# Kernel optimization log

Measured on AMD Instinct MI355X. Metric: run time of the kernel, lower is better.

## Reference

```python
import jax, jax.numpy as jnp
import numpy as np

V, E, D = 100000, 128, 60  # vocab, embedding_size, d_alpha
B, J, M, P = 512, 101, 50, 5120
EPS = 1e-6


def setup_inputs() -> dict:
    key = jax.random.key(0)
    ks = jax.random.split(key, 12)
    s = 0.5 / E
    inp = {
        'batch_titems': jax.random.randint(ks[0], (B, J), 0, V),
        'batch_citems': jax.random.randint(ks[1], (B, M), 0, V),
        'batch_pad_ids': jax.random.randint(ks[2], (2, P), 0, M),
        't_emb': jax.random.uniform(ks[3], (V, E), jnp.float32, -s, s),
        'c_emb': jax.random.uniform(ks[4], (V, E), jnp.float32, -s, s),
        'Ac_w': jax.random.normal(ks[5], (D, E), jnp.float32) * 0.05,
        'Ac_b': jnp.zeros((D,), jnp.float32),
        'At_w': jax.random.normal(ks[6], (D, E), jnp.float32) * 0.05,
        'At_b': jnp.zeros((D,), jnp.float32),
        'Bc_w': jax.random.normal(ks[7], (E, E), jnp.float32) * 0.05,
        'Bc_b': jnp.zeros((E,), jnp.float32),
        'R_w': jax.random.normal(ks[8], (E, E), jnp.float32) * 0.05,
        'R_b': jnp.zeros((E,), jnp.float32),
    }
    return inp


def reference(batch_titems, batch_citems, batch_pad_ids, t_emb, c_emb,
              Ac_w, Ac_b, At_w, At_b, Bc_w, Bc_b, R_w, R_b):
    v = t_emb[batch_titems]            # [B, J, E] target item vectors
    u = c_emb[batch_citems]            # [B, M, E] context item vectors
    tp = v @ At_w.T + At_b             # [B, J, D]
    cp = u @ Ac_w.T + Ac_b             # [B, M, D]
    # cosine similarity with torch eps clamp on norms
    dot = jnp.einsum('bjd,bmd->bjm', tp, cp)
    nt = jnp.maximum(jnp.linalg.norm(tp, axis=-1), EPS)  # [B, J]
    nc = jnp.maximum(jnp.linalg.norm(cp, axis=-1), EPS)  # [B, M]
    cos = dot / (nt[:, :, None] * nc[:, None, :])        # [B, J, M]
    # pad mask: (batch, context-pos) pairs masked across all J target rows
    mask = jnp.zeros((cos.shape[0], cos.shape[2]), bool)
    mask = mask.at[batch_pad_ids[0], batch_pad_ids[1]].set(True)
    scores = jnp.where(mask[:, None, :], -jnp.inf, cos)
    attn = jax.nn.softmax(scores, axis=-1)               # [B, J, M]
    bu = u @ Bc_w.T + Bc_b                               # [B, M, E]
    alpha = jnp.einsum('bjm,bme->bje', attn, bu)         # [B, J, E]
    return alpha @ R_w.T + R_b                           # [B, J, E]
```

## Files before the change

kernel.cpp:

```cpp
#include <hip/hip_runtime.h>

typedef unsigned short u16;
typedef unsigned int   u32;
typedef short bf8 __attribute__((ext_vector_type(8)));
typedef float f4  __attribute__((ext_vector_type(4)));

#define NB   512
#define NJ   101
#define NM   50
#define NE   128
#define ND   60
#define NP   5120
#define NT   512
#define EPSV 1e-6f

#define U_B    0
#define T_B    17408
#define C_B    33536
#define H_B    42752
#define NT2_B  61184
#define NC2_B  61632
#define MSK_B  61888
#define ARENA  62144

__device__ __forceinline__ u16 f2bh(float f) {
    return (u16)((__float_as_uint(f) + 0x8000u) >> 16);
}
__device__ __forceinline__ u32 pk2(float a, float b) {
    u32 ia = __float_as_uint(a) + 0x8000u;
    u32 ib = __float_as_uint(b) + 0x8000u;
    return (ia >> 16) | (ib & 0xFFFF0000u);
}
__device__ __forceinline__ bf8 gfrag(const float* p) {
    const float4* q = (const float4*)p;
    float4 x = q[0], y = q[1];
    union { u32 u[4]; bf8 v; } r;
    r.u[0] = pk2(x.x, x.y); r.u[1] = pk2(x.z, x.w);
    r.u[2] = pk2(y.x, y.y); r.u[3] = pk2(y.z, y.w);
    return r.v;
}

__global__ __launch_bounds__(128) void w2_kernel(
    const float* __restrict__ Bc_w, const float* __restrict__ Bc_b,
    const float* __restrict__ R_w,  const float* __restrict__ R_b,
    u16* __restrict__ w2t, float* __restrict__ rb2)
{
    const int e = blockIdx.x, k = threadIdx.x;
    const float* Rrow = R_w + e * NE;
    float a0 = 0.f, a1 = 0.f, a2 = 0.f, a3 = 0.f;
    #pragma unroll 8
    for (int j = 0; j < NE; j += 4) {
        a0 += Rrow[j]     * Bc_w[j * NE + k];
        a1 += Rrow[j + 1] * Bc_w[(j + 1) * NE + k];
        a2 += Rrow[j + 2] * Bc_w[(j + 2) * NE + k];
        a3 += Rrow[j + 3] * Bc_w[(j + 3) * NE + k];
    }
    w2t[e * NE + k] = f2bh((a0 + a1) + (a2 + a3));
    float c = Bc_b[k] * Rrow[k];
    for (int o = 32; o; o >>= 1) c += __shfl_xor(c, o, 64);
    __shared__ float part[2];
    if ((k & 63) == 0) part[k >> 6] = c;
    __syncthreads();
    if (k == 0) rb2[e] = part[0] + part[1] + R_b[e];
}

__global__ __launch_bounds__(NT, 4) void aitv_kernel(
    const int* __restrict__ titems, const int* __restrict__ citems,
    const int* __restrict__ pad_ids,
    const float* __restrict__ t_emb, const float* __restrict__ c_emb,
    const float* __restrict__ Ac_w,  const float* __restrict__ Ac_b,
    const float* __restrict__ At_w,  const float* __restrict__ At_b,
    const u16* __restrict__ w2t,     const float* __restrict__ rb2g,
    float* __restrict__ out)
{
    const int b    = blockIdx.x;
    const int t    = threadIdx.x;
    const int wid  = t >> 6;
    const int lane = t & 63;
    const int l15  = lane & 15;
    const int quad = lane >> 4;

    __shared__ __align__(16) char arena[ARENA];
    u16*   us16 = (u16*)(arena + U_B);   u32* us32 = (u32*)(arena + U_B);
    u16*   tp16 = (u16*)(arena + T_B);   u16* at16 = (u16*)(arena + T_B);
    u16*   cp16 = (u16*)(arena + C_B);
    u16*   hT16 = (u16*)(arena + H_B);
    float* nt2  = (float*)(arena + NT2_B);
    float* nc2  = (float*)(arena + NC2_B);
    int*   msk  = (int*)(arena + MSK_B);

    for (int i = t; i < 64 * 64; i += NT) {
        int row = i >> 6, c2 = i & 63;
        u32 val = 0;
        if (row < NM) {
            int idx = citems[b * NM + row];
            float2 x = *(const float2*)(c_emb + (size_t)idx * NE + 2 * c2);
            val = pk2(x.x, x.y);
        }
        us32[row * 68 + c2] = val;
    }
    if (t < 112) nt2[t] = 0.f;
    else if (t < 176) nc2[t - 112] = 0.f;
    else if (t < 240) msk[t - 176] = 0;
    __syncthreads();

    for (int i = t; i < NP; i += NT)
        if (pad_ids[i] == b) msk[pad_ids[NP + i]] = 1;

    for (int g = wid; g < 11; g += 8) {
        if (g < 7) {
            const int jt = g;
            const int j  = jt * 16 + l15;
            const float* vrow = t_emb + (size_t)titems[b * NJ + ((j < NJ) ? j : NJ - 1)] * NE;
            bf8 A[4];
            #pragma unroll
            for (int ks = 0; ks < 4; ks++) A[ks] = gfrag(vrow + ks * 32 + quad * 8);
            #pragma unroll
            for (int dt = 0; dt < 4; dt++) {
                const int d = dt * 16 + l15;
                const float* arow = At_w + (size_t)((d < ND) ? d : 0) * NE;
                float bv = (d < ND) ? At_b[d] : 0.f;
                f4 acc = {bv, bv, bv, bv};
                #pragma unroll
                for (int ks = 0; ks < 4; ks++)
                    acc = __builtin_amdgcn_mfma_f32_16x16x32_bf16(
                        A[ks], gfrag(arow + ks * 32 + quad * 8), acc, 0, 0, 0);
                const int j0 = jt * 16 + quad * 4;
                #pragma unroll
                for (int r = 0; r < 4; r++) {
                    float v = acc[r];
                    tp16[(j0 + r) * 72 + d] = (d < ND) ? f2bh(v) : (u16)0;
                    float q = (d < ND) ? v * v : 0.f;
                    q += __shfl_xor(q, 1, 64); q += __shfl_xor(q, 2, 64);
                    q += __shfl_xor(q, 4, 64); q += __shfl_xor(q, 8, 64);
                    if (l15 == 0) atomicAdd(&nt2[j0 + r], q);
                }
            }
        } else {
            const int mt = g - 7;
            bf8 U[4];
            #pragma unroll
            for (int ks = 0; ks < 4; ks++)
                U[ks] = *(const bf8*)(us16 + (mt * 16 + l15) * 136 + ks * 32 + quad * 8);
            #pragma unroll
            for (int dt = 0; dt < 4; dt++) {
                const int d = dt * 16 + l15;
                const float* arow = Ac_w + (size_t)((d < ND) ? d : 0) * NE;
                float bv = (d < ND) ? Ac_b[d] : 0.f;
                f4 acc = {bv, bv, bv, bv};
                #pragma unroll
                for (int ks = 0; ks < 4; ks++)
                    acc = __builtin_amdgcn_mfma_f32_16x16x32_bf16(
                        U[ks], gfrag(arow + ks * 32 + quad * 8), acc, 0, 0, 0);
                const int m0 = mt * 16 + quad * 4;
                #pragma unroll
                for (int r = 0; r < 4; r++) {
                    float v = acc[r];
                    cp16[(m0 + r) * 72 + d] = (d < ND) ? f2bh(v) : (u16)0;
                    float q = (d < ND) ? v * v : 0.f;
                    q += __shfl_xor(q, 1, 64); q += __shfl_xor(q, 2, 64);
                    q += __shfl_xor(q, 4, 64); q += __shfl_xor(q, 8, 64);
                    if (l15 == 0) atomicAdd(&nc2[m0 + r], q);
                }
            }
        }
    }
    __syncthreads();

    for (int u = wid; u < 32; u += 8) {
        int et = u >> 2, mt = u & 3;
        const u16* wrow = w2t + (size_t)(et * 16 + l15) * NE;
        bf8 U[4];
        #pragma unroll
        for (int ks = 0; ks < 4; ks++)
            U[ks] = *(const bf8*)(us16 + (mt * 16 + l15) * 136 + ks * 32 + quad * 8);
        f4 acc = {0.f, 0.f, 0.f, 0.f};
        #pragma unroll
        for (int ks = 0; ks < 4; ks++)
            acc = __builtin_amdgcn_mfma_f32_16x16x32_bf16(
                *(const bf8*)(wrow + ks * 32 + quad * 8), U[ks], acc, 0, 0, 0);
        const int e0 = et * 16 + quad * 4;
        for (int r = 0; r < 4; r++)
            hT16[(e0 + r) * 72 + mt * 16 + l15] = f2bh(acc[r]);
    }
    if (wid < 7) {
        const int jt = wid;
        f4 S[4];
        #pragma unroll
        for (int mt = 0; mt < 4; mt++) {
            f4 acc = {0.f, 0.f, 0.f, 0.f};
            #pragma unroll
            for (int ks = 0; ks < 2; ks++) {
                bf8 a  = *(const bf8*)(tp16 + (jt * 16 + l15) * 72 + ks * 32 + quad * 8);
                bf8 bb = *(const bf8*)(cp16 + (mt * 16 + l15) * 72 + ks * 32 + quad * 8);
                acc = __builtin_amdgcn_mfma_f32_16x16x32_bf16(a, bb, acc, 0, 0, 0);
            }
            S[mt] = acc;
        }
        bool valid[4]; float ncS[4];
        #pragma unroll
        for (int mt = 0; mt < 4; mt++) {
            int m = mt * 16 + l15;
            valid[mt] = (m < NM) && (msk[m] == 0);
            ncS[mt]   = valid[mt] ? fmaxf(sqrtf(nc2[m]), EPSV) : 1.f;
        }
        #pragma unroll
        for (int r = 0; r < 4; r++) {
            int j = jt * 16 + quad * 4 + r;
            float ntj = fmaxf(sqrtf(nt2[j]), EPSV);
            float x[4], mx = -INFINITY;
            #pragma unroll
            for (int mt = 0; mt < 4; mt++) {
                x[mt] = valid[mt] ? S[mt][r] / (ntj * ncS[mt]) : -INFINITY;
                mx = fmaxf(mx, x[mt]);
            }
            mx = fmaxf(mx, __shfl_xor(mx, 1, 64)); mx = fmaxf(mx, __shfl_xor(mx, 2, 64));
            mx = fmaxf(mx, __shfl_xor(mx, 4, 64)); mx = fmaxf(mx, __shfl_xor(mx, 8, 64));
            float p[4], sm = 0.f;
            #pragma unroll
            for (int mt = 0; mt < 4; mt++) {
                p[mt] = valid[mt] ? __expf(x[mt] - mx) : 0.f;
                sm += p[mt];
            }
            sm += __shfl_xor(sm, 1, 64); sm += __shfl_xor(sm, 2, 64);
            sm += __shfl_xor(sm, 4, 64); sm += __shfl_xor(sm, 8, 64);
            float inv = (sm > 0.f) ? 1.f / sm : 0.f;
            #pragma unroll
            for (int mt = 0; mt < 4; mt++)
                at16[j * 72 + mt * 16 + l15] = f2bh(p[mt] * inv);
        }
    }
    __syncthreads();

    for (int u = wid; u < 56; u += 8) {
        int jt = u >> 3, et = u & 7;
        float bv = rb2g[et * 16 + l15];
        f4 acc = {bv, bv, bv, bv};
        #pragma unroll
        for (int ks = 0; ks < 2; ks++) {
            bf8 a  = *(const bf8*)(at16 + (jt * 16 + l15) * 72 + ks * 32 + quad * 8);
            bf8 bb = *(const bf8*)(hT16 + (et * 16 + l15) * 72 + ks * 32 + quad * 8);
            acc = __builtin_amdgcn_mfma_f32_16x16x32_bf16(a, bb, acc, 0, 0, 0);
        }
        int e = et * 16 + l15, j0 = jt * 16 + quad * 4;
        for (int r = 0; r < 4; r++) {
            int j = j0 + r;
            if (j < NJ) out[((size_t)b * NJ + j) * NE + e] = acc[r];
        }
    }
}

extern "C" void kernel_launch(void* const* d_in, const int* in_sizes, int n_in,
                              void* d_out, int out_size, void* d_ws, size_t ws_size,
                              hipStream_t stream) {
    const int*   titems  = (const int*)d_in[0];
    const int*   citems  = (const int*)d_in[1];
    const int*   pad_ids = (const int*)d_in[2];
    const float* t_emb   = (const float*)d_in[3];
    const float* c_emb   = (const float*)d_in[4];
    const float* Ac_w    = (const float*)d_in[5];
    const float* Ac_b    = (const float*)d_in[6];
    const float* At_w    = (const float*)d_in[7];
    const float* At_b    = (const float*)d_in[8];
    const float* Bc_w    = (const float*)d_in[9];
    const float* Bc_b    = (const float*)d_in[10];
    const float* R_w     = (const float*)d_in[11];
    const float* R_b     = (const float*)d_in[12];
    float* out = (float*)d_out;

    u16*   w2t = (u16*)d_ws;
    float* rb2 = (float*)((char*)d_ws + 32768);

    w2_kernel<<<NE, NE, 0, stream>>>(Bc_w, Bc_b, R_w, R_b, w2t, rb2);
    aitv_kernel<<<NB, NT, 0, stream>>>(titems, citems, pad_ids, t_emb, c_emb,
                                       Ac_w, Ac_b, At_w, At_b, w2t, rb2, out);
}
```

Before: 181.1 us.

## Double block threads, pre-convert projection weights to bf16, and rebalance MFMA work across waves

```diff
diff --git a/kernel.cpp b/kernel.cpp
--- a/kernel.cpp
+++ b/kernel.cpp
@@ -11,7 +11,7 @@
 #define NE   128
 #define ND   60
 #define NP   5120
-#define NT   512
+#define NT   1024
 #define EPSV 1e-6f
 
 #define U_B    0
@@ -31,9 +31,7 @@
     u32 ib = __float_as_uint(b) + 0x8000u;
     return (ia >> 16) | (ib & 0xFFFF0000u);
 }
-__device__ __forceinline__ bf8 gfrag(const float* p) {
-    const float4* q = (const float4*)p;
-    float4 x = q[0], y = q[1];
+__device__ __forceinline__ bf8 pkfrag(float4 x, float4 y) {
     union { u32 u[4]; bf8 v; } r;
     r.u[0] = pk2(x.x, x.y); r.u[1] = pk2(x.z, x.w);
     r.u[2] = pk2(y.x, y.y); r.u[3] = pk2(y.z, y.w);
@@ -43,7 +41,9 @@
 __global__ __launch_bounds__(128) void w2_kernel(
     const float* __restrict__ Bc_w, const float* __restrict__ Bc_b,
     const float* __restrict__ R_w,  const float* __restrict__ R_b,
-    u16* __restrict__ w2t, float* __restrict__ rb2)
+    const float* __restrict__ At_w, const float* __restrict__ Ac_w,
+    u16* __restrict__ w2t, float* __restrict__ rb2,
+    u16* __restrict__ atw, u16* __restrict__ acw)
 {
     const int e = blockIdx.x, k = threadIdx.x;
     const float* Rrow = R_w + e * NE;
@@ -56,6 +56,10 @@
         a3 += Rrow[j + 3] * Bc_w[(j + 3) * NE + k];
     }
     w2t[e * NE + k] = f2bh((a0 + a1) + (a2 + a3));
+    if (e < ND) {
+        atw[e * NE + k] = f2bh(At_w[e * NE + k]);
+        acw[e * NE + k] = f2bh(Ac_w[e * NE + k]);
+    }
     float c = Bc_b[k] * Rrow[k];
     for (int o = 32; o; o >>= 1) c += __shfl_xor(c, o, 64);
     __shared__ float part[2];
@@ -64,12 +68,33 @@
     if (k == 0) rb2[e] = part[0] + part[1] + R_b[e];
 }
 
-__global__ __launch_bounds__(NT, 4) void aitv_kernel(
+__device__ __forceinline__ void ht_unit(int h, int l15, int quad,
+    const u16* __restrict__ us16, const u16* __restrict__ w2t,
+    u16* __restrict__ hT16)
+{
+    const int et = h >> 2, mt = h & 3;
+    const u16* wrow = w2t + (size_t)(et * 16 + l15) * NE;
+    bf8 U[4];
+    #pragma unroll
+    for (int ks = 0; ks < 4; ks++)
+        U[ks] = *(const bf8*)(us16 + (mt * 16 + l15) * 136 + ks * 32 + quad * 8);
+    f4 acc = {0.f, 0.f, 0.f, 0.f};
+    #pragma unroll
+    for (int ks = 0; ks < 4; ks++)
+        acc = __builtin_amdgcn_mfma_f32_16x16x32_bf16(
+            *(const bf8*)(wrow + ks * 32 + quad * 8), U[ks], acc, 0, 0, 0);
+    const int e0 = et * 16 + quad * 4;
+    #pragma unroll
+    for (int r = 0; r < 4; r++)
+        hT16[(e0 + r) * 72 + mt * 16 + l15] = f2bh(acc[r]);
+}
+
+__global__ __launch_bounds__(NT, 8) void aitv_kernel(
     const int* __restrict__ titems, const int* __restrict__ citems,
     const int* __restrict__ pad_ids,
     const float* __restrict__ t_emb, const float* __restrict__ c_emb,
-    const float* __restrict__ Ac_w,  const float* __restrict__ Ac_b,
-    const float* __restrict__ At_w,  const float* __restrict__ At_b,
+    const u16* __restrict__ atw,     const float* __restrict__ At_b,
+    const u16* __restrict__ acw,     const float* __restrict__ Ac_b,
     const u16* __restrict__ w2t,     const float* __restrict__ rb2g,
     float* __restrict__ out)
 {
@@ -89,42 +114,58 @@
     float* nc2  = (float*)(arena + NC2_B);
     int*   msk  = (int*)(arena + MSK_B);
 
-    for (int i = t; i < 64 * 64; i += NT) {
-        int row = i >> 6, c2 = i & 63;
+    float4 px[8];
+    const int jt_w = wid >> 1;
+    if (wid < 14) {
+        int j = jt_w * 16 + l15; if (j > NJ - 1) j = NJ - 1;
+        const float* vrow = t_emb + (size_t)titems[b * NJ + j] * NE + quad * 8;
+        #pragma unroll
+        for (int ks = 0; ks < 4; ks++) {
+            px[2 * ks]     = *(const float4*)(vrow + ks * 32);
+            px[2 * ks + 1] = *(const float4*)(vrow + ks * 32 + 4);
+        }
+    }
+
+    #pragma unroll
+    for (int i = 0; i < 4; i++) {
+        int row = wid + i * 16;
         u32 val = 0;
         if (row < NM) {
             int idx = citems[b * NM + row];
-            float2 x = *(const float2*)(c_emb + (size_t)idx * NE + 2 * c2);
+            float2 x = *(const float2*)(c_emb + (size_t)idx * NE + 2 * lane);
             val = pk2(x.x, x.y);
         }
-        us32[row * 68 + c2] = val;
+        us32[row * 68 + lane] = val;
     }
     if (t < 112) nt2[t] = 0.f;
     else if (t < 176) nc2[t - 112] = 0.f;
     else if (t < 240) msk[t - 176] = 0;
+
+    bf8 A[4];
+    if (wid < 14) {
+        #pragma unroll
+        for (int ks = 0; ks < 4; ks++) A[ks] = pkfrag(px[2 * ks], px[2 * ks + 1]);
+    }
     __syncthreads();
 
     for (int i = t; i < NP; i += NT)
         if (pad_ids[i] == b) msk[pad_ids[NP + i]] = 1;
 
-    for (int g = wid; g < 11; g += 8) {
-        if (g < 7) {
-            const int jt = g;
-            const int j  = jt * 16 + l15;
-            const float* vrow = t_emb + (size_t)titems[b * NJ + ((j < NJ) ? j : NJ - 1)] * NE;
-            bf8 A[4];
-            #pragma unroll
-            for (int ks = 0; ks < 4; ks++) A[ks] = gfrag(vrow + ks * 32 + quad * 8);
-            #pragma unroll
-            for (int dt = 0; dt < 4; dt++) {
+    for (int g = wid; g < 36; g += 16) {
+        if (g < 14) {
+            const int jt = g >> 1;
+            const int d0 = (g & 1) * 2;
+            #pragma unroll
+            for (int dt2 = 0; dt2 < 2; dt2++) {
+                const int dt = d0 + dt2;
                 const int d = dt * 16 + l15;
-                const float* arow = At_w + (size_t)((d < ND) ? d : 0) * NE;
+                const u16* arow = atw + (size_t)((d < ND) ? d : 0) * NE;
                 float bv = (d < ND) ? At_b[d] : 0.f;
                 f4 acc = {bv, bv, bv, bv};
                 #pragma unroll
                 for (int ks = 0; ks < 4; ks++)
                     acc = __builtin_amdgcn_mfma_f32_16x16x32_bf16(
-                        A[ks], gfrag(arow + ks * 32 + quad * 8), acc, 0, 0, 0);
+                        A[ks], *(const bf8*)(arow + ks * 32 + quad * 8), acc, 0, 0, 0);
                 const int j0 = jt * 16 + quad * 4;
                 #pragma unroll
                 for (int r = 0; r < 4; r++) {
@@ -136,22 +177,25 @@
                     if (l15 == 0) atomicAdd(&nt2[j0 + r], q);
                 }
             }
-        } else {
-            const int mt = g - 7;
+        } else if (g < 22) {
+            const int c  = g - 14;
+            const int mt = c >> 1;
+            const int d0 = (c & 1) * 2;
             bf8 U[4];
             #pragma unroll
             for (int ks = 0; ks < 4; ks++)
                 U[ks] = *(const bf8*)(us16 + (mt * 16 + l15) * 136 + ks * 32 + quad * 8);
             #pragma unroll
-            for (int dt = 0; dt < 4; dt++) {
+            for (int dt2 = 0; dt2 < 2; dt2++) {
+                const int dt = d0 + dt2;
                 const int d = dt * 16 + l15;
-                const float* arow = Ac_w + (size_t)((d < ND) ? d : 0) * NE;
+                const u16* arow = acw + (size_t)((d < ND) ? d : 0) * NE;
                 float bv = (d < ND) ? Ac_b[d] : 0.f;
                 f4 acc = {bv, bv, bv, bv};
                 #pragma unroll
                 for (int ks = 0; ks < 4; ks++)
                     acc = __builtin_amdgcn_mfma_f32_16x16x32_bf16(
-                        U[ks], gfrag(arow + ks * 32 + quad * 8), acc, 0, 0, 0);
+                        U[ks], *(const bf8*)(arow + ks * 32 + quad * 8), acc, 0, 0, 0);
                 const int m0 = mt * 16 + quad * 4;
                 #pragma unroll
                 for (int r = 0; r < 4; r++) {
@@ -163,27 +207,17 @@
                     if (l15 == 0) atomicAdd(&nc2[m0 + r], q);
                 }
             }
+        } else {
+            ht_unit(g - 22, l15, quad, us16, w2t, hT16);
         }
     }
     __syncthreads();
 
-    for (int u = wid; u < 32; u += 8) {
-        int et = u >> 2, mt = u & 3;
-        const u16* wrow = w2t + (size_t)(et * 16 + l15) * NE;
-        bf8 U[4];
-        #pragma unroll
-        for (int ks = 0; ks < 4; ks++)
-            U[ks] = *(const bf8*)(us16 + (mt * 16 + l15) * 136 + ks * 32 + quad * 8);
-        f4 acc = {0.f, 0.f, 0.f, 0.f};
-        #pragma unroll
-        for (int ks = 0; ks < 4; ks++)
-            acc = __builtin_amdgcn_mfma_f32_16x16x32_bf16(
-                *(const bf8*)(wrow + ks * 32 + quad * 8), U[ks], acc, 0, 0, 0);
-        const int e0 = et * 16 + quad * 4;
-        for (int r = 0; r < 4; r++)
-            hT16[(e0 + r) * 72 + mt * 16 + l15] = f2bh(acc[r]);
-    }
-    if (wid < 7) {
+    if (wid >= 7) {
+        #pragma unroll
+        for (int k2 = 0; k2 < 2; k2++)
+            ht_unit(14 + (wid - 7) * 2 + k2, l15, quad, us16, w2t, hT16);
+    } else {
         const int jt = wid;
         f4 S[4];
         #pragma unroll
@@ -232,7 +266,7 @@
     }
     __syncthreads();
 
-    for (int u = wid; u < 56; u += 8) {
+    for (int u = wid; u < 56; u += 16) {
         int jt = u >> 3, et = u & 7;
         float bv = rb2g[et * 16 + l15];
         f4 acc = {bv, bv, bv, bv};
@@ -243,6 +277,7 @@
             acc = __builtin_amdgcn_mfma_f32_16x16x32_bf16(a, bb, acc, 0, 0, 0);
         }
         int e = et * 16 + l15, j0 = jt * 16 + quad * 4;
+        #pragma unroll
         for (int r = 0; r < 4; r++) {
             int j = j0 + r;
             if (j < NJ) out[((size_t)b * NJ + j) * NE + e] = acc[r];
@@ -270,8 +305,11 @@
 
     u16*   w2t = (u16*)d_ws;
     float* rb2 = (float*)((char*)d_ws + 32768);
-
-    w2_kernel<<<NE, NE, 0, stream>>>(Bc_w, Bc_b, R_w, R_b, w2t, rb2);
+    u16*   atw = (u16*)((char*)d_ws + 33280);
+    u16*   acw = (u16*)((char*)d_ws + 48640);
+
+    w2_kernel<<<NE, NE, 0, stream>>>(Bc_w, Bc_b, R_w, R_b, At_w, Ac_w,
+                                     w2t, rb2, atw, acw);
     aitv_kernel<<<NB, NT, 0, stream>>>(titems, citems, pad_ids, t_emb, c_emb,
-                                       Ac_w, Ac_b, At_w, At_b, w2t, rb2, out);
-}
+                                       atw, At_b, acw, Ac_b, w2t, rb2, out);
+}
```

Measured after the change: 180.9 us. About the same (-0.1%).
